# Optimization experiments

Hardware: AMD Instinct MI355X
Metric: run time of the kernel (lower is better)

Reference implementation:

```python
import jax, jax.numpy as jnp
import numpy as np

B, H, S, D = 1, 32, 2048, 128
LAST_Q = 64      # MInference uses the last 64 queries to estimate the pattern
V_TOPK = 256     # top vertical columns kept per head
S_TOPK = 512     # top slash diagonals kept per head
N_SINK = 4       # vertical columns always kept (attention sink)
N_LOCAL = 64     # local diagonals always kept
SCALE = 1.0 / np.sqrt(D)


def setup_inputs() -> dict:
    key = jax.random.key(0)
    k1, k2, k3 = jax.random.split(key, 3)
    q = jax.random.normal(k1, (B, H, S, D), jnp.float32)
    k = jax.random.normal(k2, (B, H, S, D), jnp.float32)
    v = jax.random.normal(k3, (B, H, S, D), jnp.float32)
    return {"q": q, "k": k, "v": v}


def _vertical_slash_masks(q, k):
    """Estimate per-head vertical/slash importance from the last LAST_Q queries
    and return boolean column mask [B,H,S] and diagonal mask [B,H,S]."""
    ql = q[:, :, -LAST_Q:, :]                                   # [B,H,LQ,D]
    est = jnp.einsum('bhqd,bhkd->bhqk', ql, k) * SCALE          # [B,H,LQ,S]
    rows = jnp.arange(S - LAST_Q, S)                            # global row ids
    cols = jnp.arange(S)
    causal = rows[:, None] >= cols[None, :]                     # [LQ,S]
    est = jnp.where(causal, est, -jnp.inf)
    p = jax.nn.softmax(est, axis=-1)                            # [B,H,LQ,S]

    # vertical importance: column sums of estimated attention
    vertical = p.sum(axis=2)                                    # [B,H,S]

    # slash importance: sums along diagonals d = row - col (d in [0, S-1])
    diag = jnp.clip(rows[:, None] - cols[None, :], 0, S - 1)    # negatives are causally masked (p=0)
    flat_d = diag.reshape(-1)
    flat_p = p.reshape(B * H, LAST_Q * S)
    slash = jax.vmap(lambda pr: jax.ops.segment_sum(pr, flat_d, num_segments=S))(flat_p)
    slash = slash.reshape(B, H, S)                              # [B,H,S]

    # always keep sink columns and the local diagonal band
    vertical = vertical.at[..., :N_SINK].set(jnp.inf)
    slash = slash.at[..., :N_LOCAL].set(jnp.inf)

    _, v_idx = jax.lax.top_k(vertical, V_TOPK)                  # [B,H,V_TOPK]
    _, s_idx = jax.lax.top_k(slash, S_TOPK)                     # [B,H,S_TOPK]

    scatter_true = jax.vmap(jax.vmap(lambda m, i: m.at[i].set(True)))
    vmask = scatter_true(jnp.zeros((B, H, S), bool), v_idx)     # which columns kept
    smask = scatter_true(jnp.zeros((B, H, S), bool), s_idx)     # which diagonals kept
    return vmask, smask


def reference(q, k, v):
    vmask, smask = _vertical_slash_masks(q, k)

    rows = jnp.arange(S)
    cols = jnp.arange(S)
    causal = rows[:, None] >= cols[None, :]                     # [S,S]
    d = jnp.clip(rows[:, None] - cols[None, :], 0, S - 1)       # [S,S] diagonal id

    # keep (r,c) if causal AND (column c is a top vertical OR diagonal r-c is a top slash)
    keep = causal[None, None] & (vmask[:, :, None, :] | jnp.take(smask, d, axis=-1))

    scores = jnp.einsum('bhqd,bhkd->bhqk', q, k) * SCALE        # [B,H,S,S]
    scores = jnp.where(keep, scores, -jnp.inf)
    probs = jax.nn.softmax(scores, axis=-1)                     # every row keeps diagonal 0 -> no all-masked rows
    return jnp.einsum('bhqk,bhkd->bhqd', probs, v)
```

## Files before the change

### kernel.cpp

```cpp
#include <hip/hip_runtime.h>
#include <hip/hip_bf16.h>

#define S_LEN 2048
#define NH 32
#define D_DIM 128
#define LAST_Q 64
#define SCALE_F 0.08838834764831845f
#define QSCALE (0.08838834764831845f * 1.4426950408889634f)
#define RESCALE_THR 11.54f

typedef __attribute__((ext_vector_type(8))) short bf16x8;
typedef __attribute__((ext_vector_type(4))) float f32x4;
typedef unsigned long long u64;
typedef unsigned int u32;
typedef unsigned short u16;

static __device__ __forceinline__ u16 f32_bf16(float f) {
  u32 u = __float_as_uint(f);
  u32 r = (u + 0x7FFFu + ((u >> 16) & 1u)) >> 16;
  return (u16)r;
}

static __device__ __forceinline__ u32 cvt_pk_bf16(float lo, float hi) {
  u32 r;
  asm("v_cvt_pk_bf16_f32 %0, %1, %2" : "=v"(r) : "v"(lo), "v"(hi));
  return r;
}

__global__ __launch_bounds__(256) void conv_kernel(const float* __restrict__ k,
                                                   const float* __restrict__ v,
                                                   u16* __restrict__ kpre,
                                                   u16* __restrict__ vpre) {
  int bid = blockIdx.x;
  int t = bid & 31, h = bid >> 5;
  int tid = threadIdx.x;
  int c0 = t * 64;
  __shared__ u16 Vb[64][136];
  for (int i = tid; i < 512; i += 256) {
    int r = i >> 3, s = i & 7;
    const float* srcp = v + ((size_t)(h * S_LEN + c0 + r)) * D_DIM + s * 16;
    float4 f0 = *(const float4*)(srcp);
    float4 f1 = *(const float4*)(srcp + 4);
    float4 f2 = *(const float4*)(srcp + 8);
    float4 f3 = *(const float4*)(srcp + 12);
    bf16x8 t0, t1;
    t0[0] = (short)f32_bf16(f0.x); t0[1] = (short)f32_bf16(f0.y);
    t0[2] = (short)f32_bf16(f0.z); t0[3] = (short)f32_bf16(f0.w);
    t0[4] = (short)f32_bf16(f1.x); t0[5] = (short)f32_bf16(f1.y);
    t0[6] = (short)f32_bf16(f1.z); t0[7] = (short)f32_bf16(f1.w);
    t1[0] = (short)f32_bf16(f2.x); t1[1] = (short)f32_bf16(f2.y);
    t1[2] = (short)f32_bf16(f2.z); t1[3] = (short)f32_bf16(f2.w);
    t1[4] = (short)f32_bf16(f3.x); t1[5] = (short)f32_bf16(f3.y);
    t1[6] = (short)f32_bf16(f3.z); t1[7] = (short)f32_bf16(f3.w);
    *(bf16x8*)&Vb[r][s * 16] = t0;
    *(bf16x8*)&Vb[r][s * 16 + 8] = t1;
  }
  u16* kp = kpre + (size_t)h * 262144 + (size_t)t * 8192;
#pragma unroll
  for (int j = 0; j < 4; ++j) {
    int p = j * 256 + tid;
    int r = p >> 4;
    int g = (p & 15) ^ (r & 15);
    const float* srcp = k + ((size_t)(h * S_LEN + c0 + r)) * D_DIM + g * 8;
    float4 a = *(const float4*)srcp;
    float4 b = *(const float4*)(srcp + 4);
    bf16x8 o;
    o[0] = (short)f32_bf16(a.x); o[1] = (short)f32_bf16(a.y);
    o[2] = (short)f32_bf16(a.z); o[3] = (short)f32_bf16(a.w);
    o[4] = (short)f32_bf16(b.x); o[5] = (short)f32_bf16(b.y);
    o[6] = (short)f32_bf16(b.z); o[7] = (short)f32_bf16(b.w);
    *(bf16x8*)(kp + p * 8) = o;
  }
  __syncthreads();
  u16* vp = vpre + (size_t)h * 262144 + (size_t)t * 8192;
#pragma unroll
  for (int j = 0; j < 4; ++j) {
    int p = j * 256 + tid;
    int d = p >> 3;
    int cb = (p & 7) ^ (d & 7);
    bf16x8 g;
#pragma unroll
    for (int e = 0; e < 8; ++e) g[e] = (short)Vb[cb * 8 + e][d];
    *(bf16x8*)(vp + p * 8) = g;
  }
}

__global__ __launch_bounds__(256) void est_kernel(const float* __restrict__ q,
                                                  const float* __restrict__ k,
                                                  float* __restrict__ scores) {
  int cc = blockIdx.x;
  int h = blockIdx.y;
  int tid = threadIdx.x;
  int ty = tid >> 4, tx = tid & 15;
  __shared__ float Qs[64][36];
  __shared__ float Ks[64][36];
  float acc[4][4];
#pragma unroll
  for (int i = 0; i < 4; ++i)
#pragma unroll
    for (int j = 0; j < 4; ++j) acc[i][j] = 0.f;
  const float* qbase = q + ((size_t)h * S_LEN + (S_LEN - LAST_Q)) * D_DIM;
  const float* kbase = k + ((size_t)h * S_LEN + cc * 64) * D_DIM;
  for (int dc = 0; dc < 4; ++dc) {
    __syncthreads();
    for (int i = tid; i < 512; i += 256) {
      int r = i >> 3, s = i & 7;
      float4 a = *(const float4*)(qbase + (size_t)r * D_DIM + dc * 32 + s * 4);
      *(float4*)&Qs[r][s * 4] = a;
      float4 b = *(const float4*)(kbase + (size_t)r * D_DIM + dc * 32 + s * 4);
      *(float4*)&Ks[r][s * 4] = b;
    }
    __syncthreads();
#pragma unroll
    for (int d4 = 0; d4 < 8; ++d4) {
      float4 qv[4], kv[4];
#pragma unroll
      for (int i = 0; i < 4; ++i) qv[i] = *(const float4*)&Qs[ty + 16 * i][d4 * 4];
#pragma unroll
      for (int j = 0; j < 4; ++j) kv[j] = *(const float4*)&Ks[tx + 16 * j][d4 * 4];
#pragma unroll
      for (int i = 0; i < 4; ++i)
#pragma unroll
        for (int j = 0; j < 4; ++j)
          acc[i][j] += qv[i].x * kv[j].x + qv[i].y * kv[j].y + qv[i].z * kv[j].z + qv[i].w * kv[j].w;
    }
  }
#pragma unroll
  for (int i = 0; i < 4; ++i) {
    int rl = ty + 16 * i;
    int rg = (S_LEN - LAST_Q) + rl;
#pragma unroll
    for (int j = 0; j < 4; ++j) {
      int cg = cc * 64 + tx + 16 * j;
      float vv = (cg <= rg) ? acc[i][j] * SCALE_F : -1e30f;
      scores[((size_t)h * LAST_Q + rl) * S_LEN + cg] = vv;
    }
  }
}

__global__ __launch_bounds__(256) void soft_partial_kernel(const float* __restrict__ scores,
                                                           float* __restrict__ part) {
  int h = blockIdx.x, rg = blockIdx.y;
  int tid = threadIdx.x;
  int wave = tid >> 6, lane = tid & 63;
  __shared__ float vs[2048];
  __shared__ float ss[2048];
  __shared__ float red[4];
  int i0 = tid * 8;
#pragma unroll
  for (int e = 0; e < 8; ++e) { vs[i0 + e] = 0.f; ss[i0 + e] = 0.f; }
  for (int rr = 0; rr < 8; ++rr) {
    int r = rg * 8 + rr;
    const float* sp = scores + ((size_t)h * LAST_Q + r) * S_LEN;
    float4 a = *(const float4*)(sp + i0);
    float4 b = *(const float4*)(sp + i0 + 4);
    float x[8] = {a.x, a.y, a.z, a.w, b.x, b.y, b.z, b.w};
    float wm = -1e30f;
#pragma unroll
    for (int e = 0; e < 8; ++e) wm = fmaxf(wm, x[e]);
#pragma unroll
    for (int mk = 1; mk < 64; mk <<= 1) wm = fmaxf(wm, __shfl_xor(wm, mk, 64));
    __syncthreads();
    if (lane == 0) red[wave] = wm;
    __syncthreads();
    float m = fmaxf(fmaxf(red[0], red[1]), fmaxf(red[2], red[3]));
    float psum = 0.f;
#pragma unroll
    for (int e = 0; e < 8; ++e) { x[e] = __expf(x[e] - m); psum += x[e]; }
#pragma unroll
    for (int mk = 1; mk < 64; mk <<= 1) psum += __shfl_xor(psum, mk, 64);
    __syncthreads();
    if (lane == 0) red[wave] = psum;
    __syncthreads();
    float inv = 1.f / (red[0] + red[1] + red[2] + red[3]);
    int rgl = (S_LEN - LAST_Q) + r;
#pragma unroll
    for (int e = 0; e < 8; ++e) {
      float p = x[e] * inv;
      int i = i0 + e;
      vs[i] += p;
      int d = rgl - i;
      if (d >= 0) ss[d] += p;
    }
  }
  __syncthreads();
  float* pb = part + ((size_t)(h * 8 + rg)) * 4096;
#pragma unroll
  for (int e = 0; e < 8; ++e) { pb[i0 + e] = vs[i0 + e]; pb[2048 + i0 + e] = ss[i0 + e]; }
}

__global__ __launch_bounds__(256) void topk_kernel(const float* __restrict__ part,
                                                   u64* __restrict__ vbits,
                                                   u64* __restrict__ sbits) {
  int h = blockIdx.x;
  int which = blockIdx.y;
  u64* dst = which ? (sbits + h * 32) : (vbits + h * 32);
  u32 K = which ? 512u : 256u;
  int ninf = which ? 64 : 4;
  int tid = threadIdx.x;
  int lane = tid & 63, wid = tid >> 6;
  __shared__ u32 keys[2048];
  __shared__ u32 hist[256];
  __shared__ u32 wpart[4];
  __shared__ u32 sh_pref, sh_kth;
  __shared__ u64 mbw[32];
  int i0 = tid * 8;
  float accv[8] = {0.f, 0.f, 0.f, 0.f, 0.f, 0.f, 0.f, 0.f};
  for (int rg = 0; rg < 8; ++rg) {
    const float* pp = part + ((size_t)(h * 8 + rg)) * 4096 + which * 2048 + i0;
    float4 a = *(const float4*)pp;
    float4 b = *(const float4*)(pp + 4);
    accv[0] += a.x; accv[1] += a.y; accv[2] += a.z; accv[3] += a.w;
    accv[4] += b.x; accv[5] += b.y; accv[6] += b.z; accv[7] += b.w;
  }
#pragma unroll
  for (int e = 0; e < 8; ++e) {
    int i = i0 + e;
    keys[i] = (i < ninf) ? 0x7F800000u : __float_as_uint(accv[e]);
  }
  __syncthreads();
  u32 prefix = 0;
  u32 kth = K;
  for (int shift = 24; shift >= 0; shift -= 8) {
    hist[tid] = 0;
    __syncthreads();
#pragma unroll
    for (int e = 0; e < 8; ++e) {
      u32 kk = keys[i0 + e];
      if (shift == 24 || (kk >> (shift + 8)) == (prefix >> (shift + 8)))
        atomicAdd(&hist[(kk >> shift) & 255], 1u);
    }
    __syncthreads();
    u32 v = hist[tid];
    u32 x = v;
#pragma unroll
    for (int off = 1; off < 64; off <<= 1) {
      u32 o = __shfl_up(x, off, 64);
      if (lane >= off) x += o;
    }
    if (lane == 63) wpart[wid] = x;
    __syncthreads();
    u32 base = 0;
    for (int w2 = 0; w2 < wid; ++w2) base += wpart[w2];
    u32 T = wpart[0] + wpart[1] + wpart[2] + wpart[3];
    u32 Pincl = x + base;
    u32 Sb = T - Pincl + v;
    u32 Sn = T - Pincl;
    if (Sb >= kth && Sn < kth) {
      sh_pref = prefix | ((u32)tid << shift);
      sh_kth = kth - Sn;
    }
    __syncthreads();
    prefix = sh_pref;
    kth = sh_kth;
    __syncthreads();
  }
  u32 t = prefix;
  u32 cnt = 0;
#pragma unroll
  for (int e = 0; e < 8; ++e) cnt += (keys[i0 + e] == t) ? 1u : 0u;
  u32 x = cnt;
#pragma unroll
  for (int off = 1; off < 64; off <<= 1) {
    u32 o = __shfl_up(x, off, 64);
    if (lane >= off) x += o;
  }
  if (lane == 63) wpart[wid] = x;
  __syncthreads();
  u32 base = 0;
  for (int w2 = 0; w2 < wid; ++w2) base += wpart[w2];
  u32 exc = x + base - cnt;
  unsigned char myb = 0;
  u32 seen = 0;
#pragma unroll
  for (int e = 0; e < 8; ++e) {
    u32 kk = keys[i0 + e];
    bool in = (kk > t) || (kk == t && (exc + seen) < kth);
    if (kk == t) ++seen;
    myb |= (in ? 1u : 0u) << e;
  }
  ((unsigned char*)mbw)[tid] = myb;
  __syncthreads();
  if (tid < 32) dst[tid] = mbw[tid];
}

template <bool PRE>
__global__ __launch_bounds__(256, 4) void attn_kernel(const float* __restrict__ q,
                                                      const float* __restrict__ kk,
                                                      const float* __restrict__ vv,
                                                      const u16* __restrict__ kpre,
                                                      const u16* __restrict__ vpre,
                                                      const u64* __restrict__ vbits,
                                                      const u64* __restrict__ sbits,
                                                      float* __restrict__ out) {
  int bid = blockIdx.x;
  int u = bid & 255, s = bid >> 8;
  int h = u & 31;
  int v_ = u >> 5;
  int qt;
  switch (s) {
    case 0: qt = v_; break;
    case 1: qt = 31 - v_; break;
    case 2: qt = v_ + 16; break;
    default: qt = 15 - v_; break;
  }
  int tid = threadIdx.x;
  int wave = tid >> 6, lane = tid & 63;
  int grp = lane >> 4, ln = lane & 15;

  __shared__ u16 Ks[8192];
  __shared__ u16 Vt[8192];
  __shared__ u64 smp[34];

  if (tid < 34) smp[tid] = (tid == 0 || tid == 33) ? 0ull : sbits[h * 32 + tid - 1];

  int q0w = qt * 64 + wave * 16;
  bf16x8 qf[4];
  const float* qrow = q + ((size_t)h * S_LEN + q0w + ln) * D_DIM;
#pragma unroll
  for (int ks = 0; ks < 4; ++ks) {
    const float* p = qrow + ks * 32 + grp * 8;
    float4 a = *(const float4*)p;
    float4 b = *(const float4*)(p + 4);
    bf16x8 f;
    f[0] = (short)f32_bf16(a.x * QSCALE); f[1] = (short)f32_bf16(a.y * QSCALE);
    f[2] = (short)f32_bf16(a.z * QSCALE); f[3] = (short)f32_bf16(a.w * QSCALE);
    f[4] = (short)f32_bf16(b.x * QSCALE); f[5] = (short)f32_bf16(b.y * QSCALE);
    f[6] = (short)f32_bf16(b.z * QSCALE); f[7] = (short)f32_bf16(b.w * QSCALE);
    qf[ks] = f;
  }
  f32x4 of[8];
#pragma unroll
  for (int i = 0; i < 8; ++i) of[i] = (f32x4){0.f, 0.f, 0.f, 0.f};
  float mr = -1e30f;
  float ls = 0.f;

  const int kb0 = (ln << 7) + (((0 + grp) ^ ln) << 3);
  const int kb1 = (ln << 7) + (((4 + grp) ^ ln) << 3);
  const int kb2 = (ln << 7) + (((8 + grp) ^ ln) << 3);
  const int kb3 = (ln << 7) + (((12 + grp) ^ ln) << 3);
  const int vb0 = (ln << 6) + (((0 + grp) ^ (ln & 7)) << 3);
  const int vb1 = (ln << 6) + (((4 + grp) ^ (ln & 7)) << 3);

  const u16* kp = kpre + (size_t)h * 262144;
  const u16* vp = vpre + (size_t)h * 262144;
  const float* kfb = kk + (size_t)h * S_LEN * D_DIM;
  const float* vfb = vv + (size_t)h * S_LEN * D_DIM;
  const u64* vwp = vbits + h * 32;
  int nt = qt + 1;
  int sb_lane = (lane & 48) + ((lane & 48) >> 2);

  auto dma_k = [&](int t) {
    const u16* ksrc = kp + (size_t)t * 8192;
#pragma unroll
    for (int i = 0; i < 4; ++i) {
      int chunk = wave * 4 + i;
      __builtin_amdgcn_global_load_lds(
          (const __attribute__((address_space(1))) u32*)(const void*)(ksrc + (size_t)(chunk * 64 + lane) * 8),
          (__attribute__((address_space(3))) u32*)(void*)(&Ks[chunk * 512]), 16, 0, 0);
    }
  };
  auto dma_v = [&](int t) {
    const u16* vsrc = vp + (size_t)t * 8192;
#pragma unroll
    for (int i = 0; i < 4; ++i) {
      int chunk = wave * 4 + i;
      __builtin_amdgcn_global_load_lds(
          (const __attribute__((address_space(1))) u32*)(const void*)(vsrc + (size_t)(chunk * 64 + lane) * 8),
          (__attribute__((address_space(3))) u32*)(void*)(&Vt[chunk * 512]), 16, 0, 0);
    }
  };

  if constexpr (PRE) { dma_k(0); dma_v(0); }
  __syncthreads();

  for (int t = 0; t < nt; ++t) {
    int c0 = t * 64;
    if constexpr (!PRE) {
      for (int i = tid; i < 512; i += 256) {
        int r = i >> 3, s2 = i & 7;
        const float* srcp = kfb + (size_t)(c0 + r) * D_DIM + s2 * 16;
        float4 f0 = *(const float4*)(srcp);
        float4 f1 = *(const float4*)(srcp + 4);
        float4 f2 = *(const float4*)(srcp + 8);
        float4 f3 = *(const float4*)(srcp + 12);
        bf16x8 t0, t1;
        t0[0] = (short)f32_bf16(f0.x); t0[1] = (short)f32_bf16(f0.y);
        t0[2] = (short)f32_bf16(f0.z); t0[3] = (short)f32_bf16(f0.w);
        t0[4] = (short)f32_bf16(f1.x); t0[5] = (short)f32_bf16(f1.y);
        t0[6] = (short)f32_bf16(f1.z); t0[7] = (short)f32_bf16(f1.w);
        t1[0] = (short)f32_bf16(f2.x); t1[1] = (short)f32_bf16(f2.y);
        t1[2] = (short)f32_bf16(f2.z); t1[3] = (short)f32_bf16(f2.w);
        t1[4] = (short)f32_bf16(f3.x); t1[5] = (short)f32_bf16(f3.y);
        t1[6] = (short)f32_bf16(f3.z); t1[7] = (short)f32_bf16(f3.w);
        int cb0 = s2 * 2, cb1 = s2 * 2 + 1;
        *(bf16x8*)&Ks[r * 128 + ((cb0 ^ (r & 15)) << 3)] = t0;
        *(bf16x8*)&Ks[r * 128 + ((cb1 ^ (r & 15)) << 3)] = t1;
      }
      for (int i = tid; i < 512; i += 256) {
        int r = i >> 3, s2 = i & 7;
        const float* srcp = vfb + (size_t)(c0 + r) * D_DIM + s2 * 16;
#pragma unroll
        for (int x = 0; x < 16; x += 4) {
          float4 f4 = *(const float4*)(srcp + x);
          int d0 = s2 * 16 + x;
          float vals[4] = {f4.x, f4.y, f4.z, f4.w};
#pragma unroll
          for (int y = 0; y < 4; ++y) {
            int d = d0 + y;
            Vt[d * 64 + (((r >> 3) ^ (d & 7)) << 3) + (r & 7)] = f32_bf16(vals[y]);
          }
        }
      }
      __syncthreads();
    }

    f32x4 sfr[4];
#pragma unroll
    for (int nb = 0; nb < 4; ++nb) {
      f32x4 acc = (f32x4){0.f, 0.f, 0.f, 0.f};
      acc = __builtin_amdgcn_mfma_f32_16x16x32_bf16(*(const bf16x8*)&Ks[kb0 + nb * 2048], qf[0], acc, 0, 0, 0);
      acc = __builtin_amdgcn_mfma_f32_16x16x32_bf16(*(const bf16x8*)&Ks[kb1 + nb * 2048], qf[1], acc, 0, 0, 0);
      acc = __builtin_amdgcn_mfma_f32_16x16x32_bf16(*(const bf16x8*)&Ks[kb2 + nb * 2048], qf[2], acc, 0, 0, 0);
      acc = __builtin_amdgcn_mfma_f32_16x16x32_bf16(*(const bf16x8*)&Ks[kb3 + nb * 2048], qf[3], acc, 0, 0, 0);
      sfr[nb] = acc;
    }

    float tm = sfr[0][0];
#pragma unroll
    for (int nb = 0; nb < 4; ++nb)
#pragma unroll
      for (int jj = 0; jj < 4; ++jj) tm = fmaxf(tm, sfr[nb][jj]);
    tm = fmaxf(tm, __shfl_xor(tm, 16, 64));
    tm = fmaxf(tm, __shfl_xor(tm, 32, 64));

    if (__any(tm - mr > RESCALE_THR)) {
      float mn = fmaxf(mr, tm);
      float ex = __builtin_amdgcn_exp2f(mr - mn);
      mr = mn;
      ls *= ex;
      float e0 = __shfl(ex, sb_lane, 64);
      float e1 = __shfl(ex, sb_lane + 1, 64);
      float e2 = __shfl(ex, sb_lane + 2, 64);
      float e3 = __shfl(ex, sb_lane + 3, 64);
#pragma unroll
      for (int db = 0; db < 8; ++db) {
        of[db][0] *= e0; of[db][1] *= e1; of[db][2] *= e2; of[db][3] *= e3;
      }
    }

    int Cb = (q0w + ln) - c0 - (grp << 2);
    float rs = 0.f;
    u32 pkw[8];
    if (c0 >= q0w - 48) {
#pragma unroll
      for (int nb = 0; nb < 4; ++nb) {
        float pv[4];
#pragma unroll
        for (int jj = 0; jj < 4; ++jj) {
          bool keep = (16 * nb + jj) <= Cb;
          float p = keep ? __builtin_amdgcn_exp2f(sfr[nb][jj] - mr) : 0.f;
          rs += p;
          pv[jj] = p;
        }
        pkw[nb * 2] = cvt_pk_bf16(pv[0], pv[1]);
        pkw[nb * 2 + 1] = cvt_pk_bf16(pv[2], pv[3]);
      }
    } else {
      int b0 = Cb - 63;
      int w0i = (b0 >> 6) + 1;
      int sh = b0 & 63;
      u64 lo = smp[w0i];
      u64 hi = smp[w0i + 1];
      u64 W = (sh == 0) ? lo : ((lo >> sh) | (hi << (64 - sh)));
      u64 vword = vwp[t];
#pragma unroll
      for (int nb = 0; nb < 4; ++nb) {
        u32 vn = (u32)(vword >> (16 * nb + 4 * grp)) & 0xFu;
        u32 sn = (u32)(W >> (60 - 16 * nb)) & 0xFu;
        float pv[4];
#pragma unroll
        for (int jj = 0; jj < 4; ++jj) {
          u32 keep = ((vn >> jj) | (sn >> (3 - jj))) & 1u;
          float p = keep ? __builtin_amdgcn_exp2f(sfr[nb][jj] - mr) : 0.f;
          rs += p;
          pv[jj] = p;
        }
        pkw[nb * 2] = cvt_pk_bf16(pv[0], pv[1]);
        pkw[nb * 2 + 1] = cvt_pk_bf16(pv[2], pv[3]);
      }
    }
    rs += __shfl_xor(rs, 16, 64);
    rs += __shfl_xor(rs, 32, 64);
    ls += rs;

    if constexpr (PRE) {
      __builtin_amdgcn_sched_barrier(0);
      asm volatile("s_waitcnt vmcnt(0)" ::: "memory");
      __builtin_amdgcn_s_barrier();
      if (t + 1 < nt) dma_k(t + 1);
    }

#pragma unroll
    for (int ks2 = 0; ks2 < 2; ++ks2) {
      int sl0 = ln + ((lane & 16) << 1);
      int sl1 = sl0 + 16;
      u32 a0 = __shfl(pkw[ks2 * 4 + 0], sl0, 64);
      u32 a1 = __shfl(pkw[ks2 * 4 + 1], sl0, 64);
      u32 a2 = __shfl(pkw[ks2 * 4 + 0], sl1, 64);
      u32 a3 = __shfl(pkw[ks2 * 4 + 1], sl1, 64);
      u32 b0_ = __shfl(pkw[ks2 * 4 + 2], sl0, 64);
      u32 b1_ = __shfl(pkw[ks2 * 4 + 3], sl0, 64);
      u32 b2_ = __shfl(pkw[ks2 * 4 + 2], sl1, 64);
      u32 b3_ = __shfl(pkw[ks2 * 4 + 3], sl1, 64);
      bool hi2 = grp >= 2;
      union { u32 w[4]; bf16x8 v; } pu;
      pu.w[0] = hi2 ? b0_ : a0;
      pu.w[1] = hi2 ? b1_ : a1;
      pu.w[2] = hi2 ? b2_ : a2;
      pu.w[3] = hi2 ? b3_ : a3;
      int vb = ks2 ? vb1 : vb0;
#pragma unroll
      for (int db = 0; db < 8; ++db) {
        bf16x8 vf = *(const bf16x8*)&Vt[vb + db * 1024];
        of[db] = __builtin_amdgcn_mfma_f32_16x16x32_bf16(pu.v, vf, of[db], 0, 0, 0);
      }
    }

    if constexpr (PRE) {
      __builtin_amdgcn_sched_barrier(0);
      __builtin_amdgcn_s_barrier();
      if (t + 1 < nt) {
        dma_v(t + 1);
        asm volatile("s_waitcnt vmcnt(4)" ::: "memory");
      }
      __builtin_amdgcn_s_barrier();
    } else {
      __syncthreads();
    }
  }

  float invl = 1.f / ls;
  float i0 = __shfl(invl, sb_lane, 64);
  float i1 = __shfl(invl, sb_lane + 1, 64);
  float i2 = __shfl(invl, sb_lane + 2, 64);
  float i3 = __shfl(invl, sb_lane + 3, 64);
  float* ob = out + ((size_t)h * S_LEN + q0w) * D_DIM;
#pragma unroll
  for (int db = 0; db < 8; ++db) {
    ob[(size_t)(grp * 4 + 0) * D_DIM + db * 16 + ln] = of[db][0] * i0;
    ob[(size_t)(grp * 4 + 1) * D_DIM + db * 16 + ln] = of[db][1] * i1;
    ob[(size_t)(grp * 4 + 2) * D_DIM + db * 16 + ln] = of[db][2] * i2;
    ob[(size_t)(grp * 4 + 3) * D_DIM + db * 16 + ln] = of[db][3] * i3;
  }
}

extern "C" void kernel_launch(void* const* d_in, const int* in_sizes, int n_in,
                              void* d_out, int out_size, void* d_ws, size_t ws_size,
                              hipStream_t stream) {
  const float* q = (const float*)d_in[0];
  const float* k = (const float*)d_in[1];
  const float* v = (const float*)d_in[2];
  float* out = (float*)d_out;
  float* scores = out;
  float* part = out + 4194304;
  u64* vbits = (u64*)d_ws;
  u64* sbits = vbits + 1024;
  const size_t PRE_NEED = 16384 + 2ull * 16777216;
  bool pre = ws_size >= PRE_NEED;
  u16* kpre = (u16*)((char*)d_ws + 16384);
  u16* vpre = kpre + 8388608;

  if (pre) conv_kernel<<<1024, 256, 0, stream>>>(k, v, kpre, vpre);
  est_kernel<<<dim3(32, 32), 256, 0, stream>>>(q, k, scores);
  soft_partial_kernel<<<dim3(32, 8), 256, 0, stream>>>(scores, part);
  topk_kernel<<<dim3(32, 2), 256, 0, stream>>>(part, vbits, sbits);
  if (pre)
    attn_kernel<true><<<1024, 256, 0, stream>>>(q, k, v, kpre, vpre, vbits, sbits, out);
  else
    attn_kernel<false><<<1024, 256, 0, stream>>>(q, k, v, kpre, vpre, vbits, sbits, out);
}
```

Measured before the change: 140.9 us.

## Split KV range for long causal query tiles and merge partials in combine kernel

For the 16 longest query tiles per head, the KV loop is split into two halves run by separate blocks. The first half writes a bf16 partial output plus row max and sum; the second half writes an unnormalised fp32 output. A new combine kernel rescales and merges the two partials. This shortens the longest blocks and evens out the causal load imbalance, at the cost of an extra launch, extra memory traffic and bf16 rounding of one partial. The softmax-partial stage also doubles its row-group grid, from 8 to 16 blocks per head, for more parallelism.

```diff
diff --git a/kernel.cpp b/kernel.cpp
--- a/kernel.cpp
+++ b/kernel.cpp
@@ -149,8 +149,8 @@
   int i0 = tid * 8;
 #pragma unroll
   for (int e = 0; e < 8; ++e) { vs[i0 + e] = 0.f; ss[i0 + e] = 0.f; }
-  for (int rr = 0; rr < 8; ++rr) {
-    int r = rg * 8 + rr;
+  for (int rr = 0; rr < 4; ++rr) {
+    int r = rg * 4 + rr;
     const float* sp = scores + ((size_t)h * LAST_Q + r) * S_LEN;
     float4 a = *(const float4*)(sp + i0);
     float4 b = *(const float4*)(sp + i0 + 4);
@@ -184,7 +184,7 @@
     }
   }
   __syncthreads();
-  float* pb = part + ((size_t)(h * 8 + rg)) * 4096;
+  float* pb = part + ((size_t)(h * 16 + rg)) * 4096;
 #pragma unroll
   for (int e = 0; e < 8; ++e) { pb[i0 + e] = vs[i0 + e]; pb[2048 + i0 + e] = ss[i0 + e]; }
 }
@@ -206,8 +206,8 @@
   __shared__ u64 mbw[32];
   int i0 = tid * 8;
   float accv[8] = {0.f, 0.f, 0.f, 0.f, 0.f, 0.f, 0.f, 0.f};
-  for (int rg = 0; rg < 8; ++rg) {
-    const float* pp = part + ((size_t)(h * 8 + rg)) * 4096 + which * 2048 + i0;
+  for (int rg = 0; rg < 16; ++rg) {
+    const float* pp = part + ((size_t)(h * 16 + rg)) * 4096 + which * 2048 + i0;
     float4 a = *(const float4*)pp;
     float4 b = *(const float4*)(pp + 4);
     accv[0] += a.x; accv[1] += a.y; accv[2] += a.z; accv[3] += a.w;
@@ -292,17 +292,35 @@
                                                       const u16* __restrict__ vpre,
                                                       const u64* __restrict__ vbits,
                                                       const u64* __restrict__ sbits,
+                                                      u16* __restrict__ p0,
+                                                      float* __restrict__ mlb,
+                                                      int split,
                                                       float* __restrict__ out) {
   int bid = blockIdx.x;
-  int u = bid & 255, s = bid >> 8;
-  int h = u & 31;
-  int v_ = u >> 5;
-  int qt;
-  switch (s) {
-    case 0: qt = v_; break;
-    case 1: qt = 31 - v_; break;
-    case 2: qt = v_ + 16; break;
-    default: qt = 15 - v_; break;
+  int h, qt, t0, t1, mode;
+  if (split) {
+    int rr = bid >> 3;
+    h = (bid & 7) * 4 + (rr & 3);
+    int g = rr >> 2;
+    if (g < 32) {
+      qt = 31 - (g >> 1);
+      int ntq = qt + 1, tm = ntq >> 1;
+      if ((g & 1) == 0) { mode = 1; t0 = 0;  t1 = tm;  }
+      else              { mode = 2; t0 = tm; t1 = ntq; }
+    } else {
+      mode = 0; qt = 47 - g; t0 = 0; t1 = qt + 1;
+    }
+  } else {
+    int u = bid & 255, s = bid >> 8;
+    h = u & 31;
+    int v_ = u >> 5;
+    switch (s) {
+      case 0: qt = v_; break;
+      case 1: qt = 31 - v_; break;
+      case 2: qt = v_ + 16; break;
+      default: qt = 15 - v_; break;
+    }
+    mode = 0; t0 = 0; t1 = qt + 1;
   }
   int tid = threadIdx.x;
   int wave = tid >> 6, lane = tid & 63;
@@ -347,7 +365,6 @@
   const float* kfb = kk + (size_t)h * S_LEN * D_DIM;
   const float* vfb = vv + (size_t)h * S_LEN * D_DIM;
   const u64* vwp = vbits + h * 32;
-  int nt = qt + 1;
   int sb_lane = (lane & 48) + ((lane & 48) >> 2);
 
   auto dma_k = [&](int t) {
@@ -371,10 +388,10 @@
     }
   };
 
-  if constexpr (PRE) { dma_k(0); dma_v(0); }
+  if constexpr (PRE) { dma_k(t0); dma_v(t0); }
   __syncthreads();
 
-  for (int t = 0; t < nt; ++t) {
+  for (int t = t0; t < t1; ++t) {
     int c0 = t * 64;
     if constexpr (!PRE) {
       for (int i = tid; i < 512; i += 256) {
@@ -384,18 +401,18 @@
         float4 f1 = *(const float4*)(srcp + 4);
         float4 f2 = *(const float4*)(srcp + 8);
         float4 f3 = *(const float4*)(srcp + 12);
-        bf16x8 t0, t1;
-        t0[0] = (short)f32_bf16(f0.x); t0[1] = (short)f32_bf16(f0.y);
-        t0[2] = (short)f32_bf16(f0.z); t0[3] = (short)f32_bf16(f0.w);
-        t0[4] = (short)f32_bf16(f1.x); t0[5] = (short)f32_bf16(f1.y);
-        t0[6] = (short)f32_bf16(f1.z); t0[7] = (short)f32_bf16(f1.w);
-        t1[0] = (short)f32_bf16(f2.x); t1[1] = (short)f32_bf16(f2.y);
-        t1[2] = (short)f32_bf16(f2.z); t1[3] = (short)f32_bf16(f2.w);
-        t1[4] = (short)f32_bf16(f3.x); t1[5] = (short)f32_bf16(f3.y);
-        t1[6] = (short)f32_bf16(f3.z); t1[7] = (short)f32_bf16(f3.w);
+        bf16x8 t0v, t1v;
+        t0v[0] = (short)f32_bf16(f0.x); t0v[1] = (short)f32_bf16(f0.y);
+        t0v[2] = (short)f32_bf16(f0.z); t0v[3] = (short)f32_bf16(f0.w);
+        t0v[4] = (short)f32_bf16(f1.x); t0v[5] = (short)f32_bf16(f1.y);
+        t0v[6] = (short)f32_bf16(f1.z); t0v[7] = (short)f32_bf16(f1.w);
+        t1v[0] = (short)f32_bf16(f2.x); t1v[1] = (short)f32_bf16(f2.y);
+        t1v[2] = (short)f32_bf16(f2.z); t1v[3] = (short)f32_bf16(f2.w);
+        t1v[4] = (short)f32_bf16(f3.x); t1v[5] = (short)f32_bf16(f3.y);
+        t1v[6] = (short)f32_bf16(f3.z); t1v[7] = (short)f32_bf16(f3.w);
         int cb0 = s2 * 2, cb1 = s2 * 2 + 1;
-        *(bf16x8*)&Ks[r * 128 + ((cb0 ^ (r & 15)) << 3)] = t0;
-        *(bf16x8*)&Ks[r * 128 + ((cb1 ^ (r & 15)) << 3)] = t1;
+        *(bf16x8*)&Ks[r * 128 + ((cb0 ^ (r & 15)) << 3)] = t0v;
+        *(bf16x8*)&Ks[r * 128 + ((cb1 ^ (r & 15)) << 3)] = t1v;
       }
       for (int i = tid; i < 512; i += 256) {
         int r = i >> 3, s2 = i & 7;
@@ -498,7 +515,7 @@
       __builtin_amdgcn_sched_barrier(0);
       asm volatile("s_waitcnt vmcnt(0)" ::: "memory");
       __builtin_amdgcn_s_barrier();
-      if (t + 1 < nt) dma_k(t + 1);
+      if (t + 1 < t1) dma_k(t + 1);
     }
 
 #pragma unroll
@@ -530,7 +547,7 @@
     if constexpr (PRE) {
       __builtin_amdgcn_sched_barrier(0);
       __builtin_amdgcn_s_barrier();
-      if (t + 1 < nt) {
+      if (t + 1 < t1) {
         dma_v(t + 1);
         asm volatile("s_waitcnt vmcnt(4)" ::: "memory");
       }
@@ -540,19 +557,75 @@
     }
   }
 
-  float invl = 1.f / ls;
-  float i0 = __shfl(invl, sb_lane, 64);
-  float i1 = __shfl(invl, sb_lane + 1, 64);
-  float i2 = __shfl(invl, sb_lane + 2, 64);
-  float i3 = __shfl(invl, sb_lane + 3, 64);
-  float* ob = out + ((size_t)h * S_LEN + q0w) * D_DIM;
-#pragma unroll
-  for (int db = 0; db < 8; ++db) {
-    ob[(size_t)(grp * 4 + 0) * D_DIM + db * 16 + ln] = of[db][0] * i0;
-    ob[(size_t)(grp * 4 + 1) * D_DIM + db * 16 + ln] = of[db][1] * i1;
-    ob[(size_t)(grp * 4 + 2) * D_DIM + db * 16 + ln] = of[db][2] * i2;
-    ob[(size_t)(grp * 4 + 3) * D_DIM + db * 16 + ln] = of[db][3] * i3;
-  }
+  if (mode == 0) {
+    float invl = 1.f / ls;
+    float i0 = __shfl(invl, sb_lane, 64);
+    float i1 = __shfl(invl, sb_lane + 1, 64);
+    float i2 = __shfl(invl, sb_lane + 2, 64);
+    float i3 = __shfl(invl, sb_lane + 3, 64);
+    float* ob = out + ((size_t)h * S_LEN + q0w) * D_DIM;
+#pragma unroll
+    for (int db = 0; db < 8; ++db) {
+      ob[(size_t)(grp * 4 + 0) * D_DIM + db * 16 + ln] = of[db][0] * i0;
+      ob[(size_t)(grp * 4 + 1) * D_DIM + db * 16 + ln] = of[db][1] * i1;
+      ob[(size_t)(grp * 4 + 2) * D_DIM + db * 16 + ln] = of[db][2] * i2;
+      ob[(size_t)(grp * 4 + 3) * D_DIM + db * 16 + ln] = of[db][3] * i3;
+    }
+  } else {
+    int ro_base = q0w - 1024;
+    if (mode == 2) {
+      float* ob = out + ((size_t)h * S_LEN + q0w) * D_DIM;
+#pragma unroll
+      for (int db = 0; db < 8; ++db)
+#pragma unroll
+        for (int j = 0; j < 4; ++j)
+          ob[(size_t)(grp * 4 + j) * D_DIM + db * 16 + ln] = of[db][j];
+    } else {
+      u16* pb = p0 + ((size_t)h * 1024 + ro_base) * D_DIM;
+#pragma unroll
+      for (int db = 0; db < 8; ++db)
+#pragma unroll
+        for (int j = 0; j < 4; ++j)
+          pb[(size_t)(grp * 4 + j) * D_DIM + db * 16 + ln] = f32_bf16(of[db][j]);
+    }
+    if (lane < 16) {
+      int ro = ro_base + ln;
+      float* mb = mlb + (size_t)(mode - 1) * 65536;
+      mb[h * 1024 + ro] = mr;
+      mb[32768 + h * 1024 + ro] = ls;
+    }
+  }
+}
+
+__global__ __launch_bounds__(256) void combine_kernel(const u16* __restrict__ p0,
+                                                      const float* __restrict__ mlb,
+                                                      float* __restrict__ out) {
+  int bid = blockIdx.x;
+  int h = bid >> 6, rg = bid & 63;
+  int tid = threadIdx.x;
+  int r = rg * 16 + (tid >> 4);
+  int c = (tid & 15) * 8;
+  int idx = h * 1024 + r;
+  float M0 = mlb[idx],          L0 = mlb[32768 + idx];
+  float M1 = mlb[65536 + idx],  L1 = mlb[98304 + idx];
+  float M = fmaxf(M0, M1);
+  float w0 = __builtin_amdgcn_exp2f(M0 - M);
+  float w1 = __builtin_amdgcn_exp2f(M1 - M);
+  float inv = 1.f / (L0 * w0 + L1 * w1);
+  size_t po = ((size_t)h * 1024 + r) * 128 + c;
+  size_t oo = ((size_t)h * 2048 + 1024 + r) * 128 + c;
+  bf16x8 a = *(const bf16x8*)(p0 + po);
+  float4 b0 = *(const float4*)(out + oo);
+  float4 b1 = *(const float4*)(out + oo + 4);
+  float bvals[8] = {b0.x, b0.y, b0.z, b0.w, b1.x, b1.y, b1.z, b1.w};
+  float o[8];
+#pragma unroll
+  for (int e = 0; e < 8; ++e) {
+    float av = __uint_as_float(((u32)(u16)a[e]) << 16);
+    o[e] = (av * w0 + bvals[e] * w1) * inv;
+  }
+  *(float4*)(out + oo) = make_float4(o[0], o[1], o[2], o[3]);
+  *(float4*)(out + oo + 4) = make_float4(o[4], o[5], o[6], o[7]);
 }
 
 extern "C" void kernel_launch(void* const* d_in, const int* in_sizes, int n_in,
@@ -567,16 +640,29 @@
   u64* vbits = (u64*)d_ws;
   u64* sbits = vbits + 1024;
   const size_t PRE_NEED = 16384 + 2ull * 16777216;
+  const size_t SPLIT_NEED = PRE_NEED + 8388608 + 524288;
   bool pre = ws_size >= PRE_NEED;
+  bool split = ws_size >= SPLIT_NEED;
   u16* kpre = (u16*)((char*)d_ws + 16384);
   u16* vpre = kpre + 8388608;
+  u16* p0 = (u16*)((char*)d_ws + PRE_NEED);
+  float* mlb = (float*)((char*)d_ws + PRE_NEED + 8388608);
 
   if (pre) conv_kernel<<<1024, 256, 0, stream>>>(k, v, kpre, vpre);
   est_kernel<<<dim3(32, 32), 256, 0, stream>>>(q, k, scores);
-  soft_partial_kernel<<<dim3(32, 8), 256, 0, stream>>>(scores, part);
+  soft_partial_kernel<<<dim3(32, 16), 256, 0, stream>>>(scores, part);
   topk_kernel<<<dim3(32, 2), 256, 0, stream>>>(part, vbits, sbits);
-  if (pre)
-    attn_kernel<true><<<1024, 256, 0, stream>>>(q, k, v, kpre, vpre, vbits, sbits, out);
-  else
-    attn_kernel<false><<<1024, 256, 0, stream>>>(q, k, v, kpre, vpre, vbits, sbits, out);
-}
+  if (pre) {
+    if (split) {
+      attn_kernel<true><<<1536, 256, 0, stream>>>(q, k, v, kpre, vpre, vbits, sbits,
+                                                  p0, mlb, 1, out);
+      combine_kernel<<<2048, 256, 0, stream>>>(p0, mlb, out);
+    } else {
+      attn_kernel<true><<<1024, 256, 0, stream>>>(q, k, v, kpre, vpre, vbits, sbits,
+                                                  p0, mlb, 0, out);
+    }
+  } else {
+    attn_kernel<false><<<1024, 256, 0, stream>>>(q, k, v, kpre, vpre, vbits, sbits,
+                                                 p0, mlb, 0, out);
+  }
+}
```

Result: slower. 155.6 us (+10.5%).

## Double-buffer K/V tiles in LDS with one barrier per iteration

Applied to the files above, without the earlier changes.

Replaces the single K/V LDS buffers, which were refilled in staggered halves, with two buffers. The DMA for the next tile is issued at the start of each iteration so it can overlap the whole QK and PV compute, and the loop now needs one wait plus barrier per iteration instead of three barriers. LDS use doubles to about 64KB per block, so launch_bounds drops to 2 blocks per CU, which cuts occupancy and latency hiding.

```diff
diff --git a/kernel.cpp b/kernel.cpp
--- a/kernel.cpp
+++ b/kernel.cpp
@@ -285,7 +285,7 @@
 }
 
 template <bool PRE>
-__global__ __launch_bounds__(256, 4) void attn_kernel(const float* __restrict__ q,
+__global__ __launch_bounds__(256, 2) void attn_kernel(const float* __restrict__ q,
                                                       const float* __restrict__ kk,
                                                       const float* __restrict__ vv,
                                                       const u16* __restrict__ kpre,
@@ -308,8 +308,8 @@
   int wave = tid >> 6, lane = tid & 63;
   int grp = lane >> 4, ln = lane & 15;
 
-  __shared__ u16 Ks[8192];
-  __shared__ u16 Vt[8192];
+  __shared__ u16 Ks[2][8192];
+  __shared__ u16 Vt[2][8192];
   __shared__ u64 smp[34];
 
   if (tid < 34) smp[tid] = (tid == 0 || tid == 33) ? 0ull : sbits[h * 32 + tid - 1];
@@ -350,56 +350,56 @@
   int nt = qt + 1;
   int sb_lane = (lane & 48) + ((lane & 48) >> 2);
 
-  auto dma_k = [&](int t) {
+  auto dma_tile = [&](int t, int b) {
     const u16* ksrc = kp + (size_t)t * 8192;
+    const u16* vsrc = vp + (size_t)t * 8192;
 #pragma unroll
     for (int i = 0; i < 4; ++i) {
       int chunk = wave * 4 + i;
       __builtin_amdgcn_global_load_lds(
           (const __attribute__((address_space(1))) u32*)(const void*)(ksrc + (size_t)(chunk * 64 + lane) * 8),
-          (__attribute__((address_space(3))) u32*)(void*)(&Ks[chunk * 512]), 16, 0, 0);
-    }
-  };
-  auto dma_v = [&](int t) {
-    const u16* vsrc = vp + (size_t)t * 8192;
-#pragma unroll
-    for (int i = 0; i < 4; ++i) {
-      int chunk = wave * 4 + i;
+          (__attribute__((address_space(3))) u32*)(void*)(&Ks[b][chunk * 512]), 16, 0, 0);
       __builtin_amdgcn_global_load_lds(
           (const __attribute__((address_space(1))) u32*)(const void*)(vsrc + (size_t)(chunk * 64 + lane) * 8),
-          (__attribute__((address_space(3))) u32*)(void*)(&Vt[chunk * 512]), 16, 0, 0);
+          (__attribute__((address_space(3))) u32*)(void*)(&Vt[b][chunk * 512]), 16, 0, 0);
     }
   };
 
-  if constexpr (PRE) { dma_k(0); dma_v(0); }
+  if constexpr (PRE) {
+    dma_tile(0, 0);
+    asm volatile("s_waitcnt vmcnt(0)" ::: "memory");
+  }
   __syncthreads();
 
   for (int t = 0; t < nt; ++t) {
-    int c0 = t * 64;
-    if constexpr (!PRE) {
+    int cur = t & 1;
+    if constexpr (PRE) {
+      if (t + 1 < nt) dma_tile(t + 1, cur ^ 1);
+    } else {
+      int c0f = t * 64;
       for (int i = tid; i < 512; i += 256) {
         int r = i >> 3, s2 = i & 7;
-        const float* srcp = kfb + (size_t)(c0 + r) * D_DIM + s2 * 16;
+        const float* srcp = kfb + (size_t)(c0f + r) * D_DIM + s2 * 16;
         float4 f0 = *(const float4*)(srcp);
         float4 f1 = *(const float4*)(srcp + 4);
         float4 f2 = *(const float4*)(srcp + 8);
         float4 f3 = *(const float4*)(srcp + 12);
-        bf16x8 t0, t1;
-        t0[0] = (short)f32_bf16(f0.x); t0[1] = (short)f32_bf16(f0.y);
-        t0[2] = (short)f32_bf16(f0.z); t0[3] = (short)f32_bf16(f0.w);
-        t0[4] = (short)f32_bf16(f1.x); t0[5] = (short)f32_bf16(f1.y);
-        t0[6] = (short)f32_bf16(f1.z); t0[7] = (short)f32_bf16(f1.w);
-        t1[0] = (short)f32_bf16(f2.x); t1[1] = (short)f32_bf16(f2.y);
-        t1[2] = (short)f32_bf16(f2.z); t1[3] = (short)f32_bf16(f2.w);
-        t1[4] = (short)f32_bf16(f3.x); t1[5] = (short)f32_bf16(f3.y);
-        t1[6] = (short)f32_bf16(f3.z); t1[7] = (short)f32_bf16(f3.w);
+        bf16x8 t0v, t1v;
+        t0v[0] = (short)f32_bf16(f0.x); t0v[1] = (short)f32_bf16(f0.y);
+        t0v[2] = (short)f32_bf16(f0.z); t0v[3] = (short)f32_bf16(f0.w);
+        t0v[4] = (short)f32_bf16(f1.x); t0v[5] = (short)f32_bf16(f1.y);
+        t0v[6] = (short)f32_bf16(f1.z); t0v[7] = (short)f32_bf16(f1.w);
+        t1v[0] = (short)f32_bf16(f2.x); t1v[1] = (short)f32_bf16(f2.y);
+        t1v[2] = (short)f32_bf16(f2.z); t1v[3] = (short)f32_bf16(f2.w);
+        t1v[4] = (short)f32_bf16(f3.x); t1v[5] = (short)f32_bf16(f3.y);
+        t1v[6] = (short)f32_bf16(f3.z); t1v[7] = (short)f32_bf16(f3.w);
         int cb0 = s2 * 2, cb1 = s2 * 2 + 1;
-        *(bf16x8*)&Ks[r * 128 + ((cb0 ^ (r & 15)) << 3)] = t0;
-        *(bf16x8*)&Ks[r * 128 + ((cb1 ^ (r & 15)) << 3)] = t1;
+        *(bf16x8*)&Ks[0][r * 128 + ((cb0 ^ (r & 15)) << 3)] = t0v;
+        *(bf16x8*)&Ks[0][r * 128 + ((cb1 ^ (r & 15)) << 3)] = t1v;
       }
       for (int i = tid; i < 512; i += 256) {
         int r = i >> 3, s2 = i & 7;
-        const float* srcp = vfb + (size_t)(c0 + r) * D_DIM + s2 * 16;
+        const float* srcp = vfb + (size_t)(c0f + r) * D_DIM + s2 * 16;
 #pragma unroll
         for (int x = 0; x < 16; x += 4) {
           float4 f4 = *(const float4*)(srcp + x);
@@ -408,21 +408,26 @@
 #pragma unroll
           for (int y = 0; y < 4; ++y) {
             int d = d0 + y;
-            Vt[d * 64 + (((r >> 3) ^ (d & 7)) << 3) + (r & 7)] = f32_bf16(vals[y]);
+            Vt[0][d * 64 + (((r >> 3) ^ (d & 7)) << 3) + (r & 7)] = f32_bf16(vals[y]);
           }
         }
       }
+      cur = 0;
       __syncthreads();
     }
+
+    const u16* Kc = Ks[cur];
+    const u16* Vc = Vt[cur];
+    int c0 = t * 64;
 
     f32x4 sfr[4];
 #pragma unroll
     for (int nb = 0; nb < 4; ++nb) {
       f32x4 acc = (f32x4){0.f, 0.f, 0.f, 0.f};
-      acc = __builtin_amdgcn_mfma_f32_16x16x32_bf16(*(const bf16x8*)&Ks[kb0 + nb * 2048], qf[0], acc, 0, 0, 0);
-      acc = __builtin_amdgcn_mfma_f32_16x16x32_bf16(*(const bf16x8*)&Ks[kb1 + nb * 2048], qf[1], acc, 0, 0, 0);
-      acc = __builtin_amdgcn_mfma_f32_16x16x32_bf16(*(const bf16x8*)&Ks[kb2 + nb * 2048], qf[2], acc, 0, 0, 0);
-      acc = __builtin_amdgcn_mfma_f32_16x16x32_bf16(*(const bf16x8*)&Ks[kb3 + nb * 2048], qf[3], acc, 0, 0, 0);
+      acc = __builtin_amdgcn_mfma_f32_16x16x32_bf16(*(const bf16x8*)&Kc[kb0 + nb * 2048], qf[0], acc, 0, 0, 0);
+      acc = __builtin_amdgcn_mfma_f32_16x16x32_bf16(*(const bf16x8*)&Kc[kb1 + nb * 2048], qf[1], acc, 0, 0, 0);
+      acc = __builtin_amdgcn_mfma_f32_16x16x32_bf16(*(const bf16x8*)&Kc[kb2 + nb * 2048], qf[2], acc, 0, 0, 0);
+      acc = __builtin_amdgcn_mfma_f32_16x16x32_bf16(*(const bf16x8*)&Kc[kb3 + nb * 2048], qf[3], acc, 0, 0, 0);
       sfr[nb] = acc;
     }
 
@@ -493,13 +498,6 @@
     rs += __shfl_xor(rs, 16, 64);
     rs += __shfl_xor(rs, 32, 64);
     ls += rs;
-
-    if constexpr (PRE) {
-      __builtin_amdgcn_sched_barrier(0);
-      asm volatile("s_waitcnt vmcnt(0)" ::: "memory");
-      __builtin_amdgcn_s_barrier();
-      if (t + 1 < nt) dma_k(t + 1);
-    }
 
 #pragma unroll
     for (int ks2 = 0; ks2 < 2; ++ks2) {
@@ -522,19 +520,17 @@
       int vb = ks2 ? vb1 : vb0;
 #pragma unroll
       for (int db = 0; db < 8; ++db) {
-        bf16x8 vf = *(const bf16x8*)&Vt[vb + db * 1024];
+        bf16x8 vf = *(const bf16x8*)&Vc[vb + db * 1024];
         of[db] = __builtin_amdgcn_mfma_f32_16x16x32_bf16(pu.v, vf, of[db], 0, 0, 0);
       }
     }
 
     if constexpr (PRE) {
-      __builtin_amdgcn_sched_barrier(0);
-      __builtin_amdgcn_s_barrier();
       if (t + 1 < nt) {
-        dma_v(t + 1);
-        asm volatile("s_waitcnt vmcnt(4)" ::: "memory");
-      }
-      __builtin_amdgcn_s_barrier();
+        __builtin_amdgcn_sched_barrier(0);
+        asm volatile("s_waitcnt vmcnt(0)" ::: "memory");
+        __builtin_amdgcn_s_barrier();
+      }
     } else {
       __syncthreads();
     }
```

Result: slower. 150.9 us (+7.1%).
